# Optimization experiments

Measured on AMD Instinct MI355X. Metric: run time of the kernel, lower is better.

Reference implementation:

```python
import jax, jax.numpy as jnp
import numpy as np

N_CAT = 100000
N_USERS = 50000
N_REL = 32
D = 64
E = 1600000
NNZ = 1000000


def setup_inputs() -> dict:
    key = jax.random.key(0)
    ks = jax.random.split(key, 8)
    category_emb = jax.random.normal(ks[0], (N_CAT, D), dtype=jnp.float32)
    user_emb = jax.random.normal(ks[1], (N_USERS, D), dtype=jnp.float32)
    edge_index = jax.random.randint(ks[2], (2, E), 0, N_CAT, dtype=jnp.int64)
    edge_type = jax.random.randint(ks[3], (E,), 1, N_REL + 1, dtype=jnp.int64)  # 1-indexed relations
    im_rows = jax.random.randint(ks[4], (NNZ,), 0, N_USERS, dtype=jnp.int64)
    im_cols = jax.random.randint(ks[5], (NNZ,), 0, N_CAT, dtype=jnp.int64)
    im_vals = jax.random.uniform(ks[6], (NNZ,), dtype=jnp.float32)
    weight = jax.random.normal(ks[7], (N_REL, D), dtype=jnp.float32)
    return {"category_emb": category_emb, "user_emb": user_emb,
            "edge_index": edge_index, "edge_type": edge_type,
            "im_rows": im_rows, "im_cols": im_cols, "im_vals": im_vals,
            "weight": weight}


def reference(category_emb, user_emb, edge_index, edge_type, im_rows, im_cols, im_vals, weight):
    n_categories = category_emb.shape[0]
    n_users = user_emb.shape[0]
    head, tail = edge_index[0], edge_index[1]

    edge_relation_emb = weight[edge_type - 1]                      # [E, D]
    neigh_relation_emb = category_emb[tail] * edge_relation_emb    # [E, D]

    # attention weight: (||h*r|| * ||t*r||)^2 per edge -> scalar per edge
    hr = jnp.linalg.norm(category_emb[head] * edge_relation_emb, axis=1)  # [E]
    tr = jnp.linalg.norm(neigh_relation_emb, axis=1)                      # [E]
    att = (hr * tr) ** 2                                                  # [E]

    # scatter_softmax over edges grouped by head node
    grp_max = jax.ops.segment_max(att, head, num_segments=n_categories)   # [N_CAT]
    e = jnp.exp(att - grp_max[head])                                      # [E]
    grp_sum = jax.ops.segment_sum(e, head, num_segments=n_categories)     # [N_CAT]
    w = e / grp_sum[head]                                                 # [E]

    # scatter_sum aggregation to heads
    category_agg = jax.ops.segment_sum(w[:, None] * neigh_relation_emb,
                                       head, num_segments=n_categories)   # [N_CAT, D]

    # sparse interact_mat @ category_emb (COO)
    user_agg = jax.ops.segment_sum(im_vals[:, None] * category_emb[im_cols],
                                   im_rows, num_segments=n_users)         # [N_USERS, D]

    score = jax.nn.softmax(user_emb @ weight.T, axis=-1)                   # [N_USERS, N_REL]
    user_agg = user_agg + (score @ weight) * user_agg
    return (category_agg, user_agg)
```

## Files before the change

### kernel.cpp

```cpp
#include <hip/hip_runtime.h>
#include <hip/hip_bf16.h>
#include <hip/hip_fp16.h>
#include <float.h>
#include <stdint.h>

#define N_CAT   100000
#define N_USERS 50000
#define N_REL   32
#define D       64
#define NEDGE   1600000
#define NNZ     1000000

#define EB_SHIFT 9
#define EB_SIZE  512
#define NBKE     ((N_CAT + EB_SIZE - 1) / EB_SIZE)
#define UB_SHIFT 8
#define UB_SIZE  256
#define NBKU     ((N_USERS + UB_SIZE - 1) / UB_SIZE)
#define NBK      (NBKE + NBKU)

#define T1   4096
#define ECAP 15360
#define UCAP 7680

#define WSTRIDE 17


__device__ __forceinline__ unsigned int pack_half2(float a, float b) {
    return (unsigned int)__half_as_ushort(__float2half_rn(a)) |
           ((unsigned int)__half_as_ushort(__float2half_rn(b)) << 16);
}

template<int F16>
__device__ __forceinline__ void load_row8(const float4* __restrict__ catv4,
                                          const uint4* __restrict__ cath4,
                                          int row, int gl, float f[8]) {
    if (F16) {
        uint4 h = cath4[(size_t)row * 8 + gl];
        const __half2* hp = (const __half2*)&h;
        float2 a = __half22float2(hp[0]);
        float2 b = __half22float2(hp[1]);
        float2 c = __half22float2(hp[2]);
        float2 d = __half22float2(hp[3]);
        f[0] = a.x; f[1] = a.y; f[2] = b.x; f[3] = b.y;
        f[4] = c.x; f[5] = c.y; f[6] = d.x; f[7] = d.y;
    } else {
        float4 a = catv4[(size_t)row * 16 + gl * 2];
        float4 b = catv4[(size_t)row * 16 + gl * 2 + 1];
        f[0] = a.x; f[1] = a.y; f[2] = a.z; f[3] = a.w;
        f[4] = b.x; f[5] = b.y; f[6] = b.z; f[7] = b.w;
    }
}

template<int W16>
__global__ __launch_bounds__(256) void norm2_kernel(
        const float* __restrict__ cat,
        const float* __restrict__ W,
        float* __restrict__ norm2,
        unsigned short* __restrict__ cath) {
    __shared__ float4 w2[N_REL * 16];
    int t = threadIdx.x;
    const float4* Wv = (const float4*)W;
    for (int i = t; i < N_REL * 16; i += 256) {
        float4 v = Wv[i];
        v.x *= v.x; v.y *= v.y; v.z *= v.z; v.w *= v.w;
        w2[i] = v;
    }
    __syncthreads();

    int node = blockIdx.x * 64 + (t >> 2);
    int q    = t & 3;
    if (node >= N_CAT) return;

    const float4* catv = (const float4*)cat;
    float acc[N_REL];
#pragma unroll
    for (int r = 0; r < N_REL; ++r) acc[r] = 0.f;

    uint2 hp[4];
#pragma unroll
    for (int c = 0; c < 4; ++c) {
        float4 xv = catv[(size_t)node * 16 + q * 4 + c];
        if (W16) {
            hp[c].x = pack_half2(xv.x, xv.y);
            hp[c].y = pack_half2(xv.z, xv.w);
        }
        xv.x *= xv.x; xv.y *= xv.y; xv.z *= xv.z; xv.w *= xv.w;
#pragma unroll
        for (int r = 0; r < N_REL; ++r) {
            float4 wv = w2[r * 16 + q * 4 + c];
            acc[r] += xv.x * wv.x + xv.y * wv.y + xv.z * wv.z + xv.w * wv.w;
        }
    }
    if (W16) {
        uint4* cv16 = (uint4*)cath;
        cv16[(size_t)node * 8 + q * 2]     = make_uint4(hp[0].x, hp[0].y, hp[1].x, hp[1].y);
        cv16[(size_t)node * 8 + q * 2 + 1] = make_uint4(hp[2].x, hp[2].y, hp[3].x, hp[3].y);
    }
#pragma unroll
    for (int r = 0; r < N_REL; ++r) {
        acc[r] += __shfl_xor(acc[r], 1);
        acc[r] += __shfl_xor(acc[r], 2);
    }
    float4* nv = (float4*)norm2;
    size_t base = (size_t)node * 8 + q * 2;
    if (q == 0) {
        nv[base]     = make_float4(acc[0],  acc[1],  acc[2],  acc[3]);
        nv[base + 1] = make_float4(acc[4],  acc[5],  acc[6],  acc[7]);
    } else if (q == 1) {
        nv[base]     = make_float4(acc[8],  acc[9],  acc[10], acc[11]);
        nv[base + 1] = make_float4(acc[12], acc[13], acc[14], acc[15]);
    } else if (q == 2) {
        nv[base]     = make_float4(acc[16], acc[17], acc[18], acc[19]);
        nv[base + 1] = make_float4(acc[20], acc[21], acc[22], acc[23]);
    } else {
        nv[base]     = make_float4(acc[24], acc[25], acc[26], acc[27]);
        nv[base + 1] = make_float4(acc[28], acc[29], acc[30], acc[31]);
    }
}

__global__ void coarse_hist_kernel(const int* __restrict__ head,
                                   const int* __restrict__ imr,
                                   int* __restrict__ ccnt) {
    __shared__ int h[NBK];
    int t = threadIdx.x;
    for (int i = t; i < NBK; i += 256) h[i] = 0;
    __syncthreads();
    int stride = gridDim.x * 256;
    for (int i = blockIdx.x * 256 + t; i < NEDGE + NNZ; i += stride) {
        if (i < NEDGE) atomicAdd(&h[head[i] >> EB_SHIFT], 1);
        else           atomicAdd(&h[NBKE + (imr[i - NEDGE] >> UB_SHIFT)], 1);
    }
    __syncthreads();
    for (int i = t; i < NBK; i += 256) if (h[i]) atomicAdd(&ccnt[i], h[i]);
}

__global__ void coarse_scan_kernel(const int* __restrict__ ccnt,
                                   int* __restrict__ cbase_e, int* __restrict__ cbase_u,
                                   int* __restrict__ ccur_e,  int* __restrict__ ccur_u,
                                   int* __restrict__ offs_e,  int* __restrict__ offs_u) {
    __shared__ int sc[256];
    int t = threadIdx.x;
    int c = (t < NBKE) ? ccnt[t] : 0;
    sc[t] = c; __syncthreads();
    for (int off = 1; off < 256; off <<= 1) {
        int v = (t >= off) ? sc[t - off] : 0; __syncthreads();
        sc[t] += v; __syncthreads();
    }
    int excl = sc[t] - c;
    if (t < NBKE) { cbase_e[t] = excl; ccur_e[t] = excl; }
    if (t == NBKE - 1) cbase_e[NBKE] = excl + c;
    __syncthreads();
    c = (t < NBKU) ? ccnt[NBKE + t] : 0;
    sc[t] = c; __syncthreads();
    for (int off = 1; off < 256; off <<= 1) {
        int v = (t >= off) ? sc[t - off] : 0; __syncthreads();
        sc[t] += v; __syncthreads();
    }
    excl = sc[t] - c;
    if (t < NBKU) { cbase_u[t] = excl; ccur_u[t] = excl; }
    if (t == NBKU - 1) cbase_u[NBKU] = excl + c;
    if (t == 0) { offs_e[N_CAT] = NEDGE; offs_u[N_USERS] = NNZ; }
}

__global__ __launch_bounds__(256) void pass1_edges_kernel(
        const int* __restrict__ head, const int* __restrict__ tail,
        const int* __restrict__ etype, int* __restrict__ ccur_e,
        int* __restrict__ sorted_ta) {
    __shared__ int cnt[256], loc[256], base[256], sc[256];
    __shared__ int stage[T1];
    __shared__ int gpos[T1];
    int t = threadIdx.x;
    int tile = blockIdx.x * T1;
    cnt[t] = 0;
    __syncthreads();
    int rec[16], bk[16];
#pragma unroll
    for (int k = 0; k < 16; ++k) {
        int i = tile + k * 256 + t;
        if (i < NEDGE) {
            int h = head[i], tl = tail[i], r = etype[i] - 1;
            bk[k]  = h >> EB_SHIFT;
            rec[k] = ((h & (EB_SIZE - 1)) << 22) | (tl << 5) | r;
            atomicAdd(&cnt[bk[k]], 1);
        } else bk[k] = -1;
    }
    __syncthreads();
    int c = cnt[t];
    sc[t] = c; __syncthreads();
    for (int off = 1; off < 256; off <<= 1) {
        int v = (t >= off) ? sc[t - off] : 0; __syncthreads();
        sc[t] += v; __syncthreads();
    }
    loc[t] = sc[t] - c;
    if (t < NBKE && c > 0) base[t] = atomicAdd(&ccur_e[t], c);
    __syncthreads();
    cnt[t] = loc[t];
    __syncthreads();
#pragma unroll
    for (int k = 0; k < 16; ++k) {
        if (bk[k] >= 0) {
            int p = atomicAdd(&cnt[bk[k]], 1);
            stage[p] = rec[k];
            gpos[p]  = base[bk[k]] + (p - loc[bk[k]]);
        }
    }
    __syncthreads();
    int nv = min(T1, NEDGE - tile);
    for (int i = t; i < nv; i += 256) sorted_ta[gpos[i]] = stage[i];
}

__global__ __launch_bounds__(256) void pass1_users_kernel(
        const int* __restrict__ imr, const int* __restrict__ imc,
        const float* __restrict__ imv, int* __restrict__ ccur_u,
        int2* __restrict__ sorted_cv) {
    __shared__ int cnt[256], loc[256], base[256], sc[256];
    __shared__ int2 stage[T1];
    __shared__ int gpos[T1];
    int t = threadIdx.x;
    int tile = blockIdx.x * T1;
    cnt[t] = 0;
    __syncthreads();
    int2 rec[16]; int bk[16];
#pragma unroll
    for (int k = 0; k < 16; ++k) {
        int i = tile + k * 256 + t;
        if (i < NNZ) {
            int rr = imr[i];
            bk[k]  = rr >> UB_SHIFT;
            rec[k] = make_int2(((rr & (UB_SIZE - 1)) << 17) | imc[i],
                               __float_as_int(imv[i]));
            atomicAdd(&cnt[bk[k]], 1);
        } else bk[k] = -1;
    }
    __syncthreads();
    int c = cnt[t];
    sc[t] = c; __syncthreads();
    for (int off = 1; off < 256; off <<= 1) {
        int v = (t >= off) ? sc[t - off] : 0; __syncthreads();
        sc[t] += v; __syncthreads();
    }
    loc[t] = sc[t] - c;
    if (t < NBKU && c > 0) base[t] = atomicAdd(&ccur_u[t], c);
    __syncthreads();
    cnt[t] = loc[t];
    __syncthreads();
#pragma unroll
    for (int k = 0; k < 16; ++k) {
        if (bk[k] >= 0) {
            int p = atomicAdd(&cnt[bk[k]], 1);
            stage[p] = rec[k];
            gpos[p]  = base[bk[k]] + (p - loc[bk[k]]);
        }
    }
    __syncthreads();
    int nv = min(T1, NNZ - tile);
    for (int i = t; i < nv; i += 256) sorted_cv[gpos[i]] = stage[i];
}

__global__ __launch_bounds__(256) void pass2_kernel(
        const int* __restrict__ cbase_e, const int* __restrict__ cbase_u,
        int* __restrict__ offs_e, int* __restrict__ offs_u,
        int* __restrict__ sorted_ta, int2* __restrict__ sorted_cv) {
    __shared__ int lds[UCAP * 2];
    __shared__ int fh[EB_SIZE + 1];
    __shared__ int sc[256];
    int t = threadIdx.x;
    int b = blockIdx.x;
    if (b < NBKE) {
        int h0 = b << EB_SHIFT;
        int start = cbase_e[b], end = cbase_e[b + 1];
        int n = min(end - start, ECAP);
        for (int i = t; i < n; i += 256) lds[i] = sorted_ta[start + i];
        fh[2 * t] = 0; fh[2 * t + 1] = 0;
        __syncthreads();
        for (int i = t; i < n; i += 256) atomicAdd(&fh[lds[i] >> 22], 1);
        __syncthreads();
        int a = fh[2 * t], b2 = fh[2 * t + 1];
        sc[t] = a + b2; __syncthreads();
        for (int off = 1; off < 256; off <<= 1) {
            int v = (t >= off) ? sc[t - off] : 0; __syncthreads();
            sc[t] += v; __syncthreads();
        }
        int pe = sc[t] - (a + b2);
        int lim = min(EB_SIZE, N_CAT - h0);
        if (2 * t     < lim) offs_e[h0 + 2 * t]     = start + pe;
        if (2 * t + 1 < lim) offs_e[h0 + 2 * t + 1] = start + pe + a;
        fh[2 * t] = pe; fh[2 * t + 1] = pe + a;
        __syncthreads();
        for (int i = t; i < n; i += 256) {
            int rec = lds[i];
            int p = atomicAdd(&fh[rec >> 22], 1);
            sorted_ta[start + p] = rec & 0x3FFFFF;
        }
    } else {
        int k = b - NBKE;
        int u0 = k << UB_SHIFT;
        int start = cbase_u[k], end = cbase_u[k + 1];
        int n = min(end - start, UCAP);
        int2* lds2 = (int2*)lds;
        for (int i = t; i < n; i += 256) lds2[i] = sorted_cv[start + i];
        fh[t] = 0;
        __syncthreads();
        for (int i = t; i < n; i += 256) atomicAdd(&fh[lds2[i].x >> 17], 1);
        __syncthreads();
        int c = fh[t];
        sc[t] = c; __syncthreads();
        for (int off = 1; off < 256; off <<= 1) {
            int v = (t >= off) ? sc[t - off] : 0; __syncthreads();
            sc[t] += v; __syncthreads();
        }
        int excl = sc[t] - c;
        int lim = min(UB_SIZE, N_USERS - u0);
        if (t < lim) offs_u[u0 + t] = start + excl;
        fh[t] = excl;
        __syncthreads();
        for (int i = t; i < n; i += 256) {
            int2 rec = lds2[i];
            int p = atomicAdd(&fh[rec.x >> 17], 1);
            sorted_cv[start + p] = make_int2(rec.x & 0x1FFFF, rec.y);
        }
    }
}

#define FMA8(ACC, WS, F, W0, W1)                                         \
    ACC[0] += WS * F[0] * W0.x;  ACC[1] += WS * F[1] * W0.y;             \
    ACC[2] += WS * F[2] * W0.z;  ACC[3] += WS * F[3] * W0.w;             \
    ACC[4] += WS * F[4] * W1.x;  ACC[5] += WS * F[5] * W1.y;             \
    ACC[6] += WS * F[6] * W1.z;  ACC[7] += WS * F[7] * W1.w;

template<int F16>
__global__ __launch_bounds__(256, 4) void cat_agg_sorted_kernel(
        const int* __restrict__ offs_e,
        const int* __restrict__ sorted_ta,
        const float* __restrict__ norm2,
        const float* __restrict__ cat,
        const uint4* __restrict__ cath4,
        const float* __restrict__ W,
        float* __restrict__ cat_agg) {
    __shared__ float4 sW4[N_REL * WSTRIDE];
    {
        const float4* Wv = (const float4*)W;
        for (int i = threadIdx.x; i < N_REL * 16; i += 256)
            sW4[(i >> 4) * WSTRIDE + (i & 15)] = Wv[i];
    }
    __syncthreads();

    const float4* catv4 = (const float4*)cat;
    int wv   = threadIdx.x >> 6;
    int lane = threadIdx.x & 63;
    int grp  = lane >> 3;
    int gl   = lane & 7;
    int h = blockIdx.x * 4 + wv;
    int start = offs_e[h];
    int end   = offs_e[h + 1];
    int deg   = end - start;

    float accA[8], accB[8];
#pragma unroll
    for (int k = 0; k < 8; ++k) { accA[k] = 0.f; accB[k] = 0.f; }

    if (deg <= 32) {
        int rec = 0;
        if (lane < deg) rec = sorted_ta[start + lane];
        int tt = rec >> 5, r = rec & 31;
        float n2t = norm2[(size_t)tt * N_REL + r];
        float n2h = norm2[(size_t)h  * N_REL + r];

        int tA0 = __shfl(rec, grp),      tB0 = __shfl(rec, 8 + grp);
        float fA0[8], fB0[8], fA1[8], fB1[8];
        load_row8<F16>(catv4, cath4, tA0 >> 5, gl, fA0);
        load_row8<F16>(catv4, cath4, tB0 >> 5, gl, fB0);
        int tA1 = 0, tB1 = 0;
        if (deg > 16) {
            tA1 = __shfl(rec, 16 + grp); tB1 = __shfl(rec, 24 + grp);
            load_row8<F16>(catv4, cath4, tA1 >> 5, gl, fA1);
            load_row8<F16>(catv4, cath4, tB1 >> 5, gl, fB1);
        }

        float att = (lane < deg) ? n2h * n2t : -FLT_MAX;
        float m = att;
        m = fmaxf(m, __shfl_xor(m, 1));
        m = fmaxf(m, __shfl_xor(m, 2));
        m = fmaxf(m, __shfl_xor(m, 4));
        m = fmaxf(m, __shfl_xor(m, 8));
        if (deg > 16) m = fmaxf(m, __shfl_xor(m, 16));
        float ex = (lane < deg) ? __expf(att - m) : 0.f;
        float ssum = ex;
        ssum += __shfl_xor(ssum, 1);
        ssum += __shfl_xor(ssum, 2);
        ssum += __shfl_xor(ssum, 4);
        ssum += __shfl_xor(ssum, 8);
        if (deg > 16) ssum += __shfl_xor(ssum, 16);
        float w = (deg > 0) ? ex / ssum : 0.f;

        float wA0 = __shfl(w, grp), wB0 = __shfl(w, 8 + grp);
        const float4* wrA0 = &sW4[(tA0 & 31) * WSTRIDE + gl * 2];
        const float4* wrB0 = &sW4[(tB0 & 31) * WSTRIDE + gl * 2];
        float4 wa00 = wrA0[0], wa01 = wrA0[1];
        float4 wb00 = wrB0[0], wb01 = wrB0[1];
        FMA8(accA, wA0, fA0, wa00, wa01)
        FMA8(accB, wB0, fB0, wb00, wb01)
        if (deg > 16) {
            float wA1 = __shfl(w, 16 + grp), wB1 = __shfl(w, 24 + grp);
            const float4* wrA1 = &sW4[(tA1 & 31) * WSTRIDE + gl * 2];
            const float4* wrB1 = &sW4[(tB1 & 31) * WSTRIDE + gl * 2];
            float4 wa10 = wrA1[0], wa11 = wrA1[1];
            float4 wb10 = wrB1[0], wb11 = wrB1[1];
            FMA8(accA, wA1, fA1, wa10, wa11)
            FMA8(accB, wB1, fB1, wb10, wb11)
        }
    } else if (deg <= 64) {
        int   rec = 0;
        float att = -FLT_MAX;
        if (lane < deg) {
            rec = sorted_ta[start + lane];
            int tt = rec >> 5, r = rec & 31;
            att = norm2[h * N_REL + r] * norm2[(size_t)tt * N_REL + r];
        }
        float m = att;
#pragma unroll
        for (int off = 32; off > 0; off >>= 1) m = fmaxf(m, __shfl_xor(m, off));
        float ex = (lane < deg) ? __expf(att - m) : 0.f;
        float ssum = ex;
#pragma unroll
        for (int off = 32; off > 0; off >>= 1) ssum += __shfl_xor(ssum, off);
        float w = (deg > 0) ? ex / ssum : 0.f;

        for (int e = 0; e < deg; e += 16) {
            int   tA = __shfl(rec, e + grp);
            float wA = __shfl(w,   e + grp);
            int   tB = __shfl(rec, e + 8 + grp);
            float wB = __shfl(w,   e + 8 + grp);
            float fA[8], fB[8];
            load_row8<F16>(catv4, cath4, tA >> 5, gl, fA);
            load_row8<F16>(catv4, cath4, tB >> 5, gl, fB);
            const float4* wrA = &sW4[(tA & 31) * WSTRIDE + gl * 2];
            const float4* wrB = &sW4[(tB & 31) * WSTRIDE + gl * 2];
            float4 wa0 = wrA[0], wa1 = wrA[1];
            float4 wb0 = wrB[0], wb1 = wrB[1];
            FMA8(accA, wA, fA, wa0, wa1)
            FMA8(accB, wB, fB, wb0, wb1)
        }
    } else {
        float m = -FLT_MAX;
        for (int j = lane; j < deg; j += 64) {
            int rec = sorted_ta[start + j];
            int tt = rec >> 5, r = rec & 31;
            m = fmaxf(m, norm2[h * N_REL + r] * norm2[(size_t)tt * N_REL + r]);
        }
#pragma unroll
        for (int off = 32; off > 0; off >>= 1) m = fmaxf(m, __shfl_xor(m, off));
        float ssum = 0.f;
        for (int j = lane; j < deg; j += 64) {
            int rec = sorted_ta[start + j];
            int tt = rec >> 5, r = rec & 31;
            ssum += __expf(norm2[h * N_REL + r] * norm2[(size_t)tt * N_REL + r] - m);
        }
#pragma unroll
        for (int off = 32; off > 0; off >>= 1) ssum += __shfl_xor(ssum, off);
        float inv = 1.f / ssum;
        for (int j0 = 0; j0 < deg; j0 += 64) {
            int n = min(64, deg - j0);
            int   rec = 0;
            float w   = 0.f;
            if (lane < n) {
                rec = sorted_ta[start + j0 + lane];
                int tt = rec >> 5, r = rec & 31;
                w = __expf(norm2[h * N_REL + r] * norm2[(size_t)tt * N_REL + r] - m) * inv;
            }
            for (int e = 0; e < n; e += 16) {
                int   tA = __shfl(rec, e + grp);
                float wA = __shfl(w,   e + grp);
                int   tB = __shfl(rec, e + 8 + grp);
                float wB = __shfl(w,   e + 8 + grp);
                float fA[8], fB[8];
                load_row8<F16>(catv4, cath4, tA >> 5, gl, fA);
                load_row8<F16>(catv4, cath4, tB >> 5, gl, fB);
                const float4* wrA = &sW4[(tA & 31) * WSTRIDE + gl * 2];
                const float4* wrB = &sW4[(tB & 31) * WSTRIDE + gl * 2];
                float4 wa0 = wrA[0], wa1 = wrA[1];
                float4 wb0 = wrB[0], wb1 = wrB[1];
                FMA8(accA, wA, fA, wa0, wa1)
                FMA8(accB, wB, fB, wb0, wb1)
            }
        }
    }

    float o[8];
#pragma unroll
    for (int k = 0; k < 8; ++k) {
        float v = accA[k] + accB[k];
        v += __shfl_xor(v, 8);
        v += __shfl_xor(v, 16);
        v += __shfl_xor(v, 32);
        o[k] = v;
    }
    if (grp == 0) {
        float4* outv = (float4*)&cat_agg[(size_t)h * D];
        outv[gl * 2]     = make_float4(o[0], o[1], o[2], o[3]);
        outv[gl * 2 + 1] = make_float4(o[4], o[5], o[6], o[7]);
    }
}

template<int F16>
__global__ __launch_bounds__(256, 4) void spmm_user_kernel(
        const int* __restrict__ offs_u,
        const int2* __restrict__ sorted_cv,
        const float* __restrict__ cat,
        const uint4* __restrict__ cath4,
        const float* __restrict__ uemb,
        const float* __restrict__ W,
        float* __restrict__ uagg) {
    __shared__ float4 sW4[N_REL * WSTRIDE];
    __shared__ float4 s_user4[4][16];
    __shared__ float  s_score[4][N_REL];
    {
        const float4* Wv = (const float4*)W;
        for (int i = threadIdx.x; i < N_REL * 16; i += 256)
            sW4[(i >> 4) * WSTRIDE + (i & 15)] = Wv[i];
    }
    __syncthreads();

    const float4* catv4 = (const float4*)cat;
    int wv   = threadIdx.x >> 6;
    int lane = threadIdx.x & 63;
    int grp  = lane >> 3;
    int gl   = lane & 7;
    int u = blockIdx.x * 4 + wv;
    int start = offs_u[u];
    int end   = offs_u[u + 1];
    int deg   = end - start;

    float accA[8], accB[8];
#pragma unroll
    for (int k = 0; k < 8; ++k) { accA[k] = 0.f; accB[k] = 0.f; }

    if (deg <= 32) {
        int my_c = 0; float my_v = 0.f;
        if (lane < deg) {
            int2 cv = sorted_cv[start + lane];
            my_c = cv.x;
            my_v = __int_as_float(cv.y);
        }
        int   cA0 = __shfl(my_c, grp),     cB0 = __shfl(my_c, 8 + grp);
        float vA0 = __shfl(my_v, grp),     vB0 = __shfl(my_v, 8 + grp);
        float fA0[8], fB0[8], fA1[8], fB1[8];
        load_row8<F16>(catv4, cath4, cA0, gl, fA0);
        load_row8<F16>(catv4, cath4, cB0, gl, fB0);
        float vA1 = 0.f, vB1 = 0.f;
        if (deg > 16) {
            int cA1 = __shfl(my_c, 16 + grp), cB1 = __shfl(my_c, 24 + grp);
            vA1 = __shfl(my_v, 16 + grp); vB1 = __shfl(my_v, 24 + grp);
            load_row8<F16>(catv4, cath4, cA1, gl, fA1);
            load_row8<F16>(catv4, cath4, cB1, gl, fB1);
#pragma unroll
            for (int k = 0; k < 8; ++k) {
                accA[k] += vA1 * fA1[k];
                accB[k] += vB1 * fB1[k];
            }
        }
#pragma unroll
        for (int k = 0; k < 8; ++k) {
            accA[k] += vA0 * fA0[k];
            accB[k] += vB0 * fB0[k];
        }
    } else {
        for (int j0 = 0; j0 < deg; j0 += 64) {
            int n = min(64, deg - j0);
            int   my_c = 0;
            float my_v = 0.f;
            if (lane < n) {
                int2 cv = sorted_cv[start + j0 + lane];
                my_c = cv.x;
                my_v = __int_as_float(cv.y);
            }
            for (int e = 0; e < n; e += 16) {
                int   cA = __shfl(my_c, e + grp);
                float vA = __shfl(my_v, e + grp);
                int   cB = __shfl(my_c, e + 8 + grp);
                float vB = __shfl(my_v, e + 8 + grp);
                float fA[8], fB[8];
                load_row8<F16>(catv4, cath4, cA, gl, fA);
                load_row8<F16>(catv4, cath4, cB, gl, fB);
#pragma unroll
                for (int k = 0; k < 8; ++k) {
                    accA[k] += vA * fA[k];
                    accB[k] += vB * fB[k];
                }
            }
        }
    }

    float acc[8];
#pragma unroll
    for (int k = 0; k < 8; ++k) {
        float v = accA[k] + accB[k];
        v += __shfl_xor(v, 8);
        v += __shfl_xor(v, 16);
        v += __shfl_xor(v, 32);
        acc[k] = v;
    }

    ((float*)s_user4[wv])[lane] = uemb[(size_t)u * D + lane];
    __syncthreads();

    if (lane < N_REL) {
        float dot = 0.f;
        const float4* wr = &sW4[lane * WSTRIDE];
#pragma unroll
        for (int i = 0; i < 16; ++i) {
            float4 a = wr[i], b = s_user4[wv][i];
            dot += a.x * b.x + a.y * b.y + a.z * b.z + a.w * b.w;
        }
        float mm = dot;
#pragma unroll
        for (int off = 16; off > 0; off >>= 1) mm = fmaxf(mm, __shfl_xor(mm, off));
        float ex = __expf(dot - mm);
        float sm = ex;
#pragma unroll
        for (int off = 16; off > 0; off >>= 1) sm += __shfl_xor(sm, off);
        s_score[wv][lane] = ex / sm;
    }
    __syncthreads();

    float p[8];
#pragma unroll
    for (int k = 0; k < 8; ++k) p[k] = 0.f;
#pragma unroll
    for (int r = 0; r < N_REL; ++r) {
        float s = s_score[wv][r];
        float4 w0 = sW4[r * WSTRIDE + gl * 2];
        float4 w1 = sW4[r * WSTRIDE + gl * 2 + 1];
        p[0] += s * w0.x; p[1] += s * w0.y; p[2] += s * w0.z; p[3] += s * w0.w;
        p[4] += s * w1.x; p[5] += s * w1.y; p[6] += s * w1.z; p[7] += s * w1.w;
    }

    if (grp == 0) {
        float4* ov = (float4*)&uagg[(size_t)u * D];
        ov[gl * 2]     = make_float4(acc[0] * (1.f + p[0]), acc[1] * (1.f + p[1]),
                                     acc[2] * (1.f + p[2]), acc[3] * (1.f + p[3]));
        ov[gl * 2 + 1] = make_float4(acc[4] * (1.f + p[4]), acc[5] * (1.f + p[5]),
                                     acc[6] * (1.f + p[6]), acc[7] * (1.f + p[7]));
    }
}

extern "C" void kernel_launch(void* const* d_in, const int* in_sizes, int n_in,
                              void* d_out, int out_size, void* d_ws, size_t ws_size,
                              hipStream_t stream) {
    const float* cat   = (const float*)d_in[0];
    const float* uemb  = (const float*)d_in[1];
    const int*   eidx  = (const int*)d_in[2];
    const int*   etype = (const int*)d_in[3];
    const int*   imr   = (const int*)d_in[4];
    const int*   imc   = (const int*)d_in[5];
    const float* imv   = (const float*)d_in[6];
    const float* W     = (const float*)d_in[7];
    const int* head = eidx;
    const int* tail = eidx + NEDGE;

    float* out     = (float*)d_out;
    float* cat_agg = out;
    float* uagg    = out + (size_t)N_CAT * D;

    float* norm2   = (float*)d_ws;
    int*   ccnt    = (int*)(norm2 + (size_t)N_CAT * N_REL);
    int*   cbase_e = ccnt + NBK;
    int*   cbase_u = cbase_e + NBKE + 1;
    int*   ccur_e  = cbase_u + NBKU + 1;
    int*   ccur_u  = ccur_e + NBKE;
    int*   offs_e  = ccur_u + NBKU;
    int*   offs_u  = offs_e + N_CAT + 1;
    int*   sorted_ta = offs_u + N_USERS + 1;
    int2*  sorted_cv = (int2*)(sorted_ta + NEDGE);

    unsigned short* cath_us =
        (unsigned short*)(((uintptr_t)(sorted_cv + NNZ) + 255) & ~(uintptr_t)255);
    size_t need = (size_t)((char*)(cath_us + (size_t)N_CAT * D) - (char*)d_ws);
    int use16 = (ws_size >= need);

    hipMemsetAsync(ccnt, 0, (size_t)NBK * sizeof(int), stream);

    coarse_hist_kernel<<<512, 256, 0, stream>>>(head, imr, ccnt);
    coarse_scan_kernel<<<1, 256, 0, stream>>>(ccnt, cbase_e, cbase_u,
                                              ccur_e, ccur_u, offs_e, offs_u);
    pass1_edges_kernel<<<(NEDGE + T1 - 1) / T1, 256, 0, stream>>>(
        head, tail, etype, ccur_e, sorted_ta);
    pass1_users_kernel<<<(NNZ + T1 - 1) / T1, 256, 0, stream>>>(
        imr, imc, imv, ccur_u, sorted_cv);
    pass2_kernel<<<NBK, 256, 0, stream>>>(cbase_e, cbase_u, offs_e, offs_u,
                                          sorted_ta, sorted_cv);
    if (use16) {
        norm2_kernel<1><<<(N_CAT + 63) / 64, 256, 0, stream>>>(cat, W, norm2, cath_us);
        cat_agg_sorted_kernel<1><<<N_CAT / 4, 256, 0, stream>>>(
            offs_e, sorted_ta, norm2, cat, (const uint4*)cath_us, W, cat_agg);
        spmm_user_kernel<1><<<N_USERS / 4, 256, 0, stream>>>(
            offs_u, sorted_cv, cat, (const uint4*)cath_us, uemb, W, uagg);
    } else {
        norm2_kernel<0><<<(N_CAT + 63) / 64, 256, 0, stream>>>(cat, W, norm2, nullptr);
        cat_agg_sorted_kernel<0><<<N_CAT / 4, 256, 0, stream>>>(
            offs_e, sorted_ta, norm2, cat, nullptr, W, cat_agg);
        spmm_user_kernel<0><<<N_USERS / 4, 256, 0, stream>>>(
            offs_u, sorted_cv, cat, nullptr, uemb, W, uagg);
    }
}
```

Measured before the change: 326.5 us.

## Drop LDS weight staging and use reduce-scatter epilogues in aggregation kernels

Both aggregation kernels stop copying the relation weight matrix into shared memory and stop calling __syncthreads; weight rows are read straight from global memory, relying on L1 caching. The final cross-group reduction becomes a reduce-scatter, so each lane ends up owning one output dimension and all 64 lanes write, instead of an all-reduce of 8 values followed by writes from 8 lanes. The user kernel now computes the softmax score per wavefront with shuffles, keeps the weight column in registers, and exchanges scores through wave-private LDS without a block barrier. The aim is less block-level setup and fewer shuffles per output. The cost is that the inner loops take weight loads through the cache rather than LDS, and register pressure rises from the 32-entry weight array.

```diff
diff --git a/kernel.cpp b/kernel.cpp
--- a/kernel.cpp
+++ b/kernel.cpp
@@ -22,8 +22,6 @@
 #define T1   4096
 #define ECAP 15360
 #define UCAP 7680
-
-#define WSTRIDE 17
 
 
 __device__ __forceinline__ unsigned int pack_half2(float a, float b) {
@@ -50,6 +48,32 @@
         f[0] = a.x; f[1] = a.y; f[2] = a.z; f[3] = a.w;
         f[4] = b.x; f[5] = b.y; f[6] = b.z; f[7] = b.w;
     }
+}
+
+__device__ __forceinline__ float reduce_scatter8(const float a[8], int lane) {
+    int b3 = (lane >> 3) & 1, b4 = (lane >> 4) & 1, b5 = (lane >> 5) & 1;
+    float r[4];
+#pragma unroll
+    for (int j = 0; j < 4; ++j) {
+        float x = b3 ? a[j] : a[j + 4];
+        float k = b3 ? a[j + 4] : a[j];
+        r[j] = k + __shfl_xor(x, 8);
+    }
+    float s[2];
+#pragma unroll
+    for (int j = 0; j < 2; ++j) {
+        float x = b4 ? r[j] : r[j + 2];
+        float k = b4 ? r[j + 2] : r[j];
+        s[j] = k + __shfl_xor(x, 16);
+    }
+    float x = b5 ? s[0] : s[1];
+    float k = b5 ? s[1] : s[0];
+    return k + __shfl_xor(x, 32);
+}
+
+__device__ __forceinline__ int dim_of_lane(int lane) {
+    int g = lane >> 3;
+    return ((lane & 7) << 3) | ((g & 1) << 2) | (g & 2) | (g >> 2);
 }
 
 template<int W16>
@@ -329,6 +353,12 @@
     ACC[4] += WS * F[4] * W1.x;  ACC[5] += WS * F[5] * W1.y;             \
     ACC[6] += WS * F[6] * W1.z;  ACC[7] += WS * F[7] * W1.w;
 
+__device__ __forceinline__ void wrow(const float* __restrict__ W, int r, int gl,
+                                     float4& w0, float4& w1) {
+    const float4* p = (const float4*)(W + (size_t)r * D) + gl * 2;
+    w0 = p[0]; w1 = p[1];
+}
+
 template<int F16>
 __global__ __launch_bounds__(256, 4) void cat_agg_sorted_kernel(
         const int* __restrict__ offs_e,
@@ -338,14 +368,6 @@
         const uint4* __restrict__ cath4,
         const float* __restrict__ W,
         float* __restrict__ cat_agg) {
-    __shared__ float4 sW4[N_REL * WSTRIDE];
-    {
-        const float4* Wv = (const float4*)W;
-        for (int i = threadIdx.x; i < N_REL * 16; i += 256)
-            sW4[(i >> 4) * WSTRIDE + (i & 15)] = Wv[i];
-    }
-    __syncthreads();
-
     const float4* catv4 = (const float4*)cat;
     int wv   = threadIdx.x >> 6;
     int lane = threadIdx.x & 63;
@@ -395,18 +417,16 @@
         float w = (deg > 0) ? ex / ssum : 0.f;
 
         float wA0 = __shfl(w, grp), wB0 = __shfl(w, 8 + grp);
-        const float4* wrA0 = &sW4[(tA0 & 31) * WSTRIDE + gl * 2];
-        const float4* wrB0 = &sW4[(tB0 & 31) * WSTRIDE + gl * 2];
-        float4 wa00 = wrA0[0], wa01 = wrA0[1];
-        float4 wb00 = wrB0[0], wb01 = wrB0[1];
+        float4 wa00, wa01, wb00, wb01;
+        wrow(W, tA0 & 31, gl, wa00, wa01);
+        wrow(W, tB0 & 31, gl, wb00, wb01);
         FMA8(accA, wA0, fA0, wa00, wa01)
         FMA8(accB, wB0, fB0, wb00, wb01)
         if (deg > 16) {
             float wA1 = __shfl(w, 16 + grp), wB1 = __shfl(w, 24 + grp);
-            const float4* wrA1 = &sW4[(tA1 & 31) * WSTRIDE + gl * 2];
-            const float4* wrB1 = &sW4[(tB1 & 31) * WSTRIDE + gl * 2];
-            float4 wa10 = wrA1[0], wa11 = wrA1[1];
-            float4 wb10 = wrB1[0], wb11 = wrB1[1];
+            float4 wa10, wa11, wb10, wb11;
+            wrow(W, tA1 & 31, gl, wa10, wa11);
+            wrow(W, tB1 & 31, gl, wb10, wb11);
             FMA8(accA, wA1, fA1, wa10, wa11)
             FMA8(accB, wB1, fB1, wb10, wb11)
         }
@@ -435,10 +455,9 @@
             float fA[8], fB[8];
             load_row8<F16>(catv4, cath4, tA >> 5, gl, fA);
             load_row8<F16>(catv4, cath4, tB >> 5, gl, fB);
-            const float4* wrA = &sW4[(tA & 31) * WSTRIDE + gl * 2];
-            const float4* wrB = &sW4[(tB & 31) * WSTRIDE + gl * 2];
-            float4 wa0 = wrA[0], wa1 = wrA[1];
-            float4 wb0 = wrB[0], wb1 = wrB[1];
+            float4 wa0, wa1, wb0, wb1;
+            wrow(W, tA & 31, gl, wa0, wa1);
+            wrow(W, tB & 31, gl, wb0, wb1);
             FMA8(accA, wA, fA, wa0, wa1)
             FMA8(accB, wB, fB, wb0, wb1)
         }
@@ -477,30 +496,20 @@
                 float fA[8], fB[8];
                 load_row8<F16>(catv4, cath4, tA >> 5, gl, fA);
                 load_row8<F16>(catv4, cath4, tB >> 5, gl, fB);
-                const float4* wrA = &sW4[(tA & 31) * WSTRIDE + gl * 2];
-                const float4* wrB = &sW4[(tB & 31) * WSTRIDE + gl * 2];
-                float4 wa0 = wrA[0], wa1 = wrA[1];
-                float4 wb0 = wrB[0], wb1 = wrB[1];
+                float4 wa0, wa1, wb0, wb1;
+                wrow(W, tA & 31, gl, wa0, wa1);
+                wrow(W, tB & 31, gl, wb0, wb1);
                 FMA8(accA, wA, fA, wa0, wa1)
                 FMA8(accB, wB, fB, wb0, wb1)
             }
         }
     }
 
-    float o[8];
-#pragma unroll
-    for (int k = 0; k < 8; ++k) {
-        float v = accA[k] + accB[k];
-        v += __shfl_xor(v, 8);
-        v += __shfl_xor(v, 16);
-        v += __shfl_xor(v, 32);
-        o[k] = v;
-    }
-    if (grp == 0) {
-        float4* outv = (float4*)&cat_agg[(size_t)h * D];
-        outv[gl * 2]     = make_float4(o[0], o[1], o[2], o[3]);
-        outv[gl * 2 + 1] = make_float4(o[4], o[5], o[6], o[7]);
-    }
+    float a[8];
+#pragma unroll
+    for (int k = 0; k < 8; ++k) a[k] = accA[k] + accB[k];
+    float tot = reduce_scatter8(a, lane);
+    cat_agg[(size_t)h * D + dim_of_lane(lane)] = tot;
 }
 
 template<int F16>
@@ -512,25 +521,21 @@
         const float* __restrict__ uemb,
         const float* __restrict__ W,
         float* __restrict__ uagg) {
-    __shared__ float4 sW4[N_REL * WSTRIDE];
-    __shared__ float4 s_user4[4][16];
-    __shared__ float  s_score[4][N_REL];
-    {
-        const float4* Wv = (const float4*)W;
-        for (int i = threadIdx.x; i < N_REL * 16; i += 256)
-            sW4[(i >> 4) * WSTRIDE + (i & 15)] = Wv[i];
-    }
-    __syncthreads();
-
+    __shared__ float s_score[4][N_REL];
     const float4* catv4 = (const float4*)cat;
     int wv   = threadIdx.x >> 6;
     int lane = threadIdx.x & 63;
     int grp  = lane >> 3;
     int gl   = lane & 7;
+    int dim  = dim_of_lane(lane);
     int u = blockIdx.x * 4 + wv;
     int start = offs_u[u];
     int end   = offs_u[u + 1];
     int deg   = end - start;
+
+    float wreg[N_REL];
+#pragma unroll
+    for (int r = 0; r < N_REL; ++r) wreg[r] = W[(size_t)r * D + dim];
 
     float accA[8], accB[8];
 #pragma unroll
@@ -592,57 +597,47 @@
         }
     }
 
-    float acc[8];
-#pragma unroll
-    for (int k = 0; k < 8; ++k) {
-        float v = accA[k] + accB[k];
-        v += __shfl_xor(v, 8);
-        v += __shfl_xor(v, 16);
-        v += __shfl_xor(v, 32);
-        acc[k] = v;
-    }
-
-    ((float*)s_user4[wv])[lane] = uemb[(size_t)u * D + lane];
-    __syncthreads();
-
-    if (lane < N_REL) {
-        float dot = 0.f;
-        const float4* wr = &sW4[lane * WSTRIDE];
+    float a[8];
+#pragma unroll
+    for (int k = 0; k < 8; ++k) a[k] = accA[k] + accB[k];
+    float tot = reduce_scatter8(a, lane);
+
+    int rel = lane & 31;
+    float dot = 0.f;
+    {
+        const float4* Wr = (const float4*)(W + (size_t)rel * D);
+        const float4* ur = (const float4*)(uemb + (size_t)u * D);
 #pragma unroll
         for (int i = 0; i < 16; ++i) {
-            float4 a = wr[i], b = s_user4[wv][i];
-            dot += a.x * b.x + a.y * b.y + a.z * b.z + a.w * b.w;
-        }
-        float mm = dot;
-#pragma unroll
-        for (int off = 16; off > 0; off >>= 1) mm = fmaxf(mm, __shfl_xor(mm, off));
-        float ex = __expf(dot - mm);
-        float sm = ex;
-#pragma unroll
-        for (int off = 16; off > 0; off >>= 1) sm += __shfl_xor(sm, off);
-        s_score[wv][lane] = ex / sm;
-    }
-    __syncthreads();
-
-    float p[8];
-#pragma unroll
-    for (int k = 0; k < 8; ++k) p[k] = 0.f;
-#pragma unroll
-    for (int r = 0; r < N_REL; ++r) {
-        float s = s_score[wv][r];
-        float4 w0 = sW4[r * WSTRIDE + gl * 2];
-        float4 w1 = sW4[r * WSTRIDE + gl * 2 + 1];
-        p[0] += s * w0.x; p[1] += s * w0.y; p[2] += s * w0.z; p[3] += s * w0.w;
-        p[4] += s * w1.x; p[5] += s * w1.y; p[6] += s * w1.z; p[7] += s * w1.w;
-    }
-
-    if (grp == 0) {
-        float4* ov = (float4*)&uagg[(size_t)u * D];
-        ov[gl * 2]     = make_float4(acc[0] * (1.f + p[0]), acc[1] * (1.f + p[1]),
-                                     acc[2] * (1.f + p[2]), acc[3] * (1.f + p[3]));
-        ov[gl * 2 + 1] = make_float4(acc[4] * (1.f + p[4]), acc[5] * (1.f + p[5]),
-                                     acc[6] * (1.f + p[6]), acc[7] * (1.f + p[7]));
-    }
+            float4 wv4 = Wr[i], uv4 = ur[i];
+            dot += wv4.x * uv4.x + wv4.y * uv4.y + wv4.z * uv4.z + wv4.w * uv4.w;
+        }
+    }
+    float mm = dot;
+    mm = fmaxf(mm, __shfl_xor(mm, 16));
+    mm = fmaxf(mm, __shfl_xor(mm, 8));
+    mm = fmaxf(mm, __shfl_xor(mm, 4));
+    mm = fmaxf(mm, __shfl_xor(mm, 2));
+    mm = fmaxf(mm, __shfl_xor(mm, 1));
+    float ex = __expf(dot - mm);
+    float sm = ex;
+    sm += __shfl_xor(sm, 16);
+    sm += __shfl_xor(sm, 8);
+    sm += __shfl_xor(sm, 4);
+    sm += __shfl_xor(sm, 2);
+    sm += __shfl_xor(sm, 1);
+    if (lane < N_REL) s_score[wv][lane] = ex / sm;
+
+    float proj = 0.f;
+    const float4* sc4 = (const float4*)s_score[wv];
+#pragma unroll
+    for (int q = 0; q < 8; ++q) {
+        float4 s4 = sc4[q];
+        proj += s4.x * wreg[4 * q]     + s4.y * wreg[4 * q + 1]
+              + s4.z * wreg[4 * q + 2] + s4.w * wreg[4 * q + 3];
+    }
+
+    uagg[(size_t)u * D + dim] = tot * (1.f + proj);
 }
 
 extern "C" void kernel_launch(void* const* d_in, const int* in_sizes, int n_in,
```

New measurement: 476.9 us. +46.0%, slower.
